# Kernel tuning notes

Hardware: AMD Instinct MI355X
Metric: run time of the kernel (lower is better)

The kernel has to match this reference:

```python
import jax, jax.numpy as jnp
import numpy as np

P = 64       # number of pathways
NV = 512     # features per pathway (nvar[i])
W = 256      # hidden width per pathway
COV = 16     # covariates
B = 2048     # batch
EPS = 1e-5   # BatchNorm eps
SLOPE = 0.2  # LeakyReLU negative slope


def _lrelu(v):
    return jnp.where(v >= 0, v, SLOPE * v)


def setup_inputs() -> dict:
    key = jax.random.key(0)
    ks = jax.random.split(key, 8)
    x = jax.random.normal(ks[0], (B, P * NV + COV), dtype=jnp.float32)
    # per-pathway weights (no bias), stacked across pathways -> grouped GEMM
    W1 = jax.random.normal(ks[1], (P, NV, W), dtype=jnp.float32) * (1.0 / np.sqrt(NV))
    W2 = jax.random.normal(ks[2], (P, W, W), dtype=jnp.float32) * (1.0 / np.sqrt(W))
    W3 = jax.random.normal(ks[3], (P, W), dtype=jnp.float32) * (1.0 / np.sqrt(W))
    gamma = jnp.ones((P,), dtype=jnp.float32)   # bn_path weight
    beta = jnp.zeros((P,), dtype=jnp.float32)   # bn_path bias
    fc_w = jax.random.normal(ks[4], (P + COV, 1), dtype=jnp.float32) * 0.05
    fc_b = jnp.full((1,), 0.001, dtype=jnp.float32)
    return {"x": x, "W1": W1, "W2": W2, "W3": W3,
            "gamma": gamma, "beta": beta, "fc_w": fc_w, "fc_b": fc_b}


def reference(x, W1, W2, W3, gamma, beta, fc_w, fc_b):
    # pathway blocks (dropout = identity in eval): grouped GEMMs over P pathways
    xp = x[:, : P * NV].reshape(B, P, NV)
    h = _lrelu(jnp.einsum('bpi,pio->bpo', xp, W1))
    h = _lrelu(jnp.einsum('bpi,pio->bpo', h, W2))
    p = _lrelu(jnp.einsum('bpi,pi->bp', h, W3))          # [B, P]
    # BatchNorm1d (training-mode batch statistics, biased variance)
    mean = p.mean(axis=0)
    var = p.var(axis=0)
    pn = (p - mean) / jnp.sqrt(var + EPS) * gamma + beta
    # global L2 (Frobenius) normalization, as torch.norm(pathway_layer, 2)
    pn = pn / jnp.linalg.norm(pn)
    # concat covariates, final linear + sigmoid
    z = jnp.concatenate([pn, x[:, P * NV: P * NV + COV]], axis=1)  # [B, P+COV]
    return jax.nn.sigmoid(z @ fc_w + fc_b)                         # [B, 1]
```

## Files before the change

### kernel.cpp

```cpp
#include <hip/hip_runtime.h>
#include <hip/hip_bf16.h>

#define PW 64
#define NV 512
#define HW 256
#define COV 16
#define BATCH 2048
#define XROW (PW * NV + COV)

typedef short s16x8 __attribute__((ext_vector_type(8)));
typedef float f32x4 __attribute__((ext_vector_type(4)));

__device__ __forceinline__ unsigned short f2bf(float f) {
    union { float f; unsigned int u; } v;
    v.f = f;
    unsigned int u = v.u;
    unsigned int r = (u + 0x7fffu + ((u >> 16) & 1u)) >> 16;
    return (unsigned short)r;
}

__device__ __forceinline__ unsigned int pack2(float a, float b) {
    __hip_bfloat162 h = __float22bfloat162_rn(float2{a, b});
    union { __hip_bfloat162 h; unsigned int u; } c;
    c.h = h;
    return c.u;
}

__global__ __launch_bounds__(256)
void transpose_all(const float* __restrict__ W1, const float* __restrict__ W2,
                   unsigned short* __restrict__ W1T, unsigned short* __restrict__ W2T) {
    __shared__ float tile[32][33];
    const float* in;
    unsigned short* out;
    int R, C, c0, r0, p;
    int bx = blockIdx.x;
    if (bx < 8192) {
        R = NV; C = HW;
        c0 = (bx & 7) * 32;
        r0 = ((bx >> 3) & 15) * 32;
        p  = bx >> 7;
        in = W1; out = W1T;
    } else {
        bx -= 8192;
        R = HW; C = HW;
        c0 = (bx & 7) * 32;
        r0 = ((bx >> 3) & 7) * 32;
        p  = bx >> 6;
        in = W2; out = W2T;
    }
    const float* ip = in + (size_t)p * R * C;
    unsigned short* op = out + (size_t)p * R * C;
    const int tx = threadIdx.x & 31;
    const int ty = threadIdx.x >> 5;
    #pragma unroll
    for (int j = 0; j < 32; j += 8)
        tile[ty + j][tx] = ip[(size_t)(r0 + ty + j) * C + c0 + tx];
    __syncthreads();
    #pragma unroll
    for (int j = 0; j < 32; j += 8)
        op[(size_t)(c0 + ty + j) * R + r0 + tx] = f2bf(tile[tx][ty + j]);
}

template<int K, bool CONV_A, bool FUSE>
__global__ __launch_bounds__(256)
void gemm_fused(const void* __restrict__ Abase, const unsigned short* __restrict__ BT,
                unsigned short* __restrict__ Hout, const float* __restrict__ W3,
                float* __restrict__ pvec, int lda, long aPs) {
    __shared__ __align__(16) unsigned short As[128][72];
    __shared__ __align__(16) unsigned short Bs[256][72];
    __shared__ float red[2][128];

    const int p   = blockIdx.z;
    const int bm0 = blockIdx.x * 128;
    const int t    = threadIdx.x;
    const int lane = t & 63;
    const int wave = t >> 6;
    const int wm  = (wave & 1) * 64;
    const int wni = wave >> 1;
    const int wn  = wni * 128;
    const int l15  = lane & 15;
    const int quad = lane >> 4;

    f32x4 acc[4][8] = {};

    const unsigned short* Bp = BT + (size_t)p * HW * K;

    for (int k0 = 0; k0 < K; k0 += 64) {
        if (CONV_A) {
            const float* Ap = (const float*)Abase + (size_t)p * aPs;
            #pragma unroll
            for (int i = 0; i < 8; ++i) {
                int idx = t + i * 256;
                int row = idx >> 4;
                int c4  = (idx & 15) * 4;
                float4 v = *(const float4*)(Ap + (size_t)(bm0 + row) * lda + k0 + c4);
                uint2 u;
                u.x = pack2(v.x, v.y);
                u.y = pack2(v.z, v.w);
                *(uint2*)&As[row][c4] = u;
            }
        } else {
            const unsigned short* Ap = (const unsigned short*)Abase + (size_t)p * aPs;
            #pragma unroll
            for (int i = 0; i < 4; ++i) {
                int idx = t + i * 256;
                int row = idx >> 3;
                int c8  = (idx & 7) * 8;
                *(s16x8*)&As[row][c8] = *(const s16x8*)(Ap + (size_t)(bm0 + row) * lda + k0 + c8);
            }
        }
        #pragma unroll
        for (int i = 0; i < 8; ++i) {
            int idx = t + i * 256;
            int row = idx >> 3;
            int c8  = (idx & 7) * 8;
            *(s16x8*)&Bs[row][c8] = *(const s16x8*)(Bp + (size_t)row * K + k0 + c8);
        }
        __syncthreads();

        #pragma unroll
        for (int kk = 0; kk < 64; kk += 32) {
            s16x8 af[4], bfr[8];
            #pragma unroll
            for (int mi = 0; mi < 4; ++mi)
                af[mi] = *(const s16x8*)&As[wm + mi * 16 + l15][kk + quad * 8];
            #pragma unroll
            for (int ni = 0; ni < 8; ++ni)
                bfr[ni] = *(const s16x8*)&Bs[wn + ni * 16 + l15][kk + quad * 8];
            #pragma unroll
            for (int mi = 0; mi < 4; ++mi)
                #pragma unroll
                for (int ni = 0; ni < 8; ++ni)
                    acc[mi][ni] = __builtin_amdgcn_mfma_f32_16x16x32_bf16(
                        af[mi], bfr[ni], acc[mi][ni], 0, 0, 0);
        }
        __syncthreads();
    }

    if (!FUSE) {
        unsigned short* Cp = Hout + (size_t)p * BATCH * HW;
        #pragma unroll
        for (int mi = 0; mi < 4; ++mi) {
            #pragma unroll
            for (int ni = 0; ni < 8; ++ni) {
                int col = wn + ni * 16 + l15;
                #pragma unroll
                for (int r = 0; r < 4; ++r) {
                    int row = bm0 + wm + mi * 16 + quad * 4 + r;
                    float v = acc[mi][ni][r];
                    v = v >= 0.f ? v : 0.2f * v;
                    Cp[(size_t)row * HW + col] = f2bf(v);
                }
            }
        }
    } else {
        float w3v[8];
        #pragma unroll
        for (int ni = 0; ni < 8; ++ni)
            w3v[ni] = W3[(size_t)p * HW + wn + ni * 16 + l15];
        float part[4][4];
        #pragma unroll
        for (int mi = 0; mi < 4; ++mi) {
            #pragma unroll
            for (int r = 0; r < 4; ++r) {
                float s = 0.f;
                #pragma unroll
                for (int ni = 0; ni < 8; ++ni) {
                    float v = acc[mi][ni][r];
                    v = v >= 0.f ? v : 0.2f * v;
                    s += v * w3v[ni];
                }
                part[mi][r] = s;
            }
        }
        #pragma unroll
        for (int off = 1; off < 16; off <<= 1)
            #pragma unroll
            for (int mi = 0; mi < 4; ++mi)
                #pragma unroll
                for (int r = 0; r < 4; ++r)
                    part[mi][r] += __shfl_xor(part[mi][r], off);
        if (l15 == 0) {
            #pragma unroll
            for (int mi = 0; mi < 4; ++mi)
                #pragma unroll
                for (int r = 0; r < 4; ++r)
                    red[wni][wm + mi * 16 + quad * 4 + r] = part[mi][r];
        }
        __syncthreads();
        if (t < 128) {
            float s = red[0][t] + red[1][t];
            s = s >= 0.f ? s : 0.2f * s;
            pvec[(size_t)p * BATCH + bm0 + t] = s;
        }
    }
}

__global__ __launch_bounds__(1024)
void stats_all(const float* __restrict__ pvec, const float* __restrict__ gamma,
               const float* __restrict__ beta, float* __restrict__ stat) {
    __shared__ float sm[64], sq[64];
    const int wave = threadIdx.x >> 6;
    const int lane = threadIdx.x & 63;
    #pragma unroll
    for (int pp = 0; pp < 4; ++pp) {
        const int p = wave * 4 + pp;
        float s = 0.f, q = 0.f;
        for (int i = lane; i < BATCH; i += 64) {
            float v = pvec[(size_t)p * BATCH + i];
            s += v; q += v * v;
        }
        #pragma unroll
        for (int off = 32; off; off >>= 1) {
            s += __shfl_down(s, off);
            q += __shfl_down(q, off);
        }
        if (lane == 0) { sm[p] = s; sq[p] = q; }
    }
    __syncthreads();
    if (threadIdx.x < 64) {
        const int p = threadIdx.x;
        float mean = sm[p] * (1.f / BATCH);
        float var  = sq[p] * (1.f / BATCH) - mean * mean;
        float invstd = rsqrtf(var + 1e-5f);
        stat[p]      = mean;
        stat[64 + p] = invstd;
        float g = gamma[p], bt = beta[p];
        float contrib = (float)BATCH * (g * g * var / (var + 1e-5f) + bt * bt);
        #pragma unroll
        for (int off = 32; off; off >>= 1) contrib += __shfl_down(contrib, off);
        if (p == 0) stat[128] = rsqrtf(contrib);
    }
}

__global__ __launch_bounds__(256)
void final_k(const float* __restrict__ pvec, const float* __restrict__ stat,
             const float* __restrict__ gamma, const float* __restrict__ beta,
             const float* __restrict__ x, const float* __restrict__ fc_w,
             const float* __restrict__ fc_b, float* __restrict__ out) {
    const int b = blockIdx.x * 256 + threadIdx.x;
    const float rn = stat[128];
    float acc = fc_b[0];
    #pragma unroll
    for (int p = 0; p < PW; ++p) {
        float pn = (pvec[(size_t)p * BATCH + b] - stat[p]) * stat[64 + p] * gamma[p] + beta[p];
        acc += pn * rn * fc_w[p];
    }
    #pragma unroll
    for (int c = 0; c < COV; ++c)
        acc += x[(size_t)b * XROW + PW * NV + c] * fc_w[PW + c];
    out[b] = 1.f / (1.f + __expf(-acc));
}

extern "C" void kernel_launch(void* const* d_in, const int* in_sizes, int n_in,
                              void* d_out, int out_size, void* d_ws, size_t ws_size,
                              hipStream_t stream) {
    const float* x     = (const float*)d_in[0];
    const float* W1    = (const float*)d_in[1];
    const float* W2    = (const float*)d_in[2];
    const float* W3    = (const float*)d_in[3];
    const float* gamma = (const float*)d_in[4];
    const float* beta  = (const float*)d_in[5];
    const float* fc_w  = (const float*)d_in[6];
    const float* fc_b  = (const float*)d_in[7];
    float* out = (float*)d_out;

    char* ws = (char*)d_ws;
    size_t off = 0;
    unsigned short* W1T = (unsigned short*)(ws + off); off += (size_t)PW * NV * HW * 2;
    unsigned short* W2T = (unsigned short*)(ws + off); off += (size_t)PW * HW * HW * 2;
    unsigned short* H1  = (unsigned short*)(ws + off); off += (size_t)PW * BATCH * HW * 2;
    float* pvec = (float*)(ws + off); off += (size_t)PW * BATCH * 4;
    float* stat = (float*)(ws + off); off += 256 * 4;

    transpose_all<<<dim3(8192 + 4096), 256, 0, stream>>>(W1, W2, W1T, W2T);

    gemm_fused<NV, true, false><<<dim3(BATCH / 128, 1, PW), 256, 0, stream>>>(
        (const void*)x, W1T, H1, nullptr, nullptr, XROW, (long)NV);

    gemm_fused<HW, false, true><<<dim3(BATCH / 128, 1, PW), 256, 0, stream>>>(
        (const void*)H1, W2T, nullptr, W3, pvec, HW, (long)BATCH * HW);

    stats_all<<<1, 1024, 0, stream>>>(pvec, gamma, beta, stat);

    final_k<<<BATCH / 256, 256, 0, stream>>>(pvec, stat, gamma, beta, x, fc_w, fc_b, out);
}
```

Measured before the change: 541.4 us.

## Fuse both pathway GEMMs into one kernel keeping H1 in shared memory

```diff
diff --git a/kernel.cpp b/kernel.cpp
--- a/kernel.cpp
+++ b/kernel.cpp
@@ -25,6 +25,8 @@
     c.h = h;
     return c.u;
 }
+
+__device__ __forceinline__ float lrelu(float v) { return v >= 0.f ? v : 0.2f * v; }
 
 __global__ __launch_bounds__(256)
 void transpose_all(const float* __restrict__ W1, const float* __restrict__ W2,
@@ -61,175 +63,169 @@
         op[(size_t)(c0 + ty + j) * R + r0 + tx] = f2bf(tile[tx][ty + j]);
 }
 
-template<int K, bool CONV_A, bool FUSE>
-__global__ __launch_bounds__(256)
-void gemm_fused(const void* __restrict__ Abase, const unsigned short* __restrict__ BT,
-                unsigned short* __restrict__ Hout, const float* __restrict__ W3,
-                float* __restrict__ pvec, int lda, long aPs) {
-    __shared__ __align__(16) unsigned short As[128][72];
+__global__ __launch_bounds__(256, 2)
+void pathway_fused(const float* __restrict__ x, const unsigned short* __restrict__ W1T,
+                   const unsigned short* __restrict__ W2T, const float* __restrict__ W3,
+                   float* __restrict__ pvec) {
+    __shared__ __align__(16) unsigned short As[64][72];
     __shared__ __align__(16) unsigned short Bs[256][72];
-    __shared__ float red[2][128];
-
-    const int p   = blockIdx.z;
-    const int bm0 = blockIdx.x * 128;
+    __shared__ __align__(16) unsigned short H1t[64][264];
+    __shared__ float red[4][64];
+
+    const int bm0 = blockIdx.x * 64;
+    const int p   = blockIdx.y;
     const int t    = threadIdx.x;
     const int lane = t & 63;
     const int wave = t >> 6;
-    const int wm  = (wave & 1) * 64;
-    const int wni = wave >> 1;
-    const int wn  = wni * 128;
+    const int wn   = wave * 64;
     const int l15  = lane & 15;
     const int quad = lane >> 4;
 
-    f32x4 acc[4][8] = {};
-
-    const unsigned short* Bp = BT + (size_t)p * HW * K;
-
-    for (int k0 = 0; k0 < K; k0 += 64) {
-        if (CONV_A) {
-            const float* Ap = (const float*)Abase + (size_t)p * aPs;
-            #pragma unroll
-            for (int i = 0; i < 8; ++i) {
+    const float* Ap          = x   + (size_t)p * NV;
+    const unsigned short* B1 = W1T + (size_t)p * HW * NV;
+    const unsigned short* B2 = W2T + (size_t)p * HW * HW;
+
+    {
+        f32x4 acc[4][4] = {};
+        for (int k0 = 0; k0 < NV; k0 += 64) {
+            #pragma unroll
+            for (int i = 0; i < 4; ++i) {
                 int idx = t + i * 256;
                 int row = idx >> 4;
                 int c4  = (idx & 15) * 4;
-                float4 v = *(const float4*)(Ap + (size_t)(bm0 + row) * lda + k0 + c4);
+                float4 v = *(const float4*)(Ap + (size_t)(bm0 + row) * XROW + k0 + c4);
                 uint2 u;
                 u.x = pack2(v.x, v.y);
                 u.y = pack2(v.z, v.w);
                 *(uint2*)&As[row][c4] = u;
             }
-        } else {
-            const unsigned short* Ap = (const unsigned short*)Abase + (size_t)p * aPs;
-            #pragma unroll
-            for (int i = 0; i < 4; ++i) {
+            #pragma unroll
+            for (int i = 0; i < 8; ++i) {
                 int idx = t + i * 256;
                 int row = idx >> 3;
                 int c8  = (idx & 7) * 8;
-                *(s16x8*)&As[row][c8] = *(const s16x8*)(Ap + (size_t)(bm0 + row) * lda + k0 + c8);
+                *(s16x8*)&Bs[row][c8] = *(const s16x8*)(B1 + (size_t)row * NV + k0 + c8);
             }
-        }
+            __syncthreads();
+            #pragma unroll
+            for (int kk = 0; kk < 64; kk += 32) {
+                s16x8 af[4], bfr[4];
+                #pragma unroll
+                for (int mi = 0; mi < 4; ++mi)
+                    af[mi] = *(const s16x8*)&As[mi * 16 + l15][kk + quad * 8];
+                #pragma unroll
+                for (int ni = 0; ni < 4; ++ni)
+                    bfr[ni] = *(const s16x8*)&Bs[wn + ni * 16 + l15][kk + quad * 8];
+                #pragma unroll
+                for (int mi = 0; mi < 4; ++mi)
+                    #pragma unroll
+                    for (int ni = 0; ni < 4; ++ni)
+                        acc[mi][ni] = __builtin_amdgcn_mfma_f32_16x16x32_bf16(
+                            af[mi], bfr[ni], acc[mi][ni], 0, 0, 0);
+            }
+            __syncthreads();
+        }
+        #pragma unroll
+        for (int mi = 0; mi < 4; ++mi)
+            #pragma unroll
+            for (int ni = 0; ni < 4; ++ni)
+                #pragma unroll
+                for (int r = 0; r < 4; ++r)
+                    H1t[mi * 16 + quad * 4 + r][wn + ni * 16 + l15] =
+                        f2bf(lrelu(acc[mi][ni][r]));
+    }
+    __syncthreads();
+
+    f32x4 acc2[4][4] = {};
+    for (int k0 = 0; k0 < HW; k0 += 64) {
         #pragma unroll
         for (int i = 0; i < 8; ++i) {
             int idx = t + i * 256;
             int row = idx >> 3;
             int c8  = (idx & 7) * 8;
-            *(s16x8*)&Bs[row][c8] = *(const s16x8*)(Bp + (size_t)row * K + k0 + c8);
+            *(s16x8*)&Bs[row][c8] = *(const s16x8*)(B2 + (size_t)row * HW + k0 + c8);
         }
         __syncthreads();
-
         #pragma unroll
         for (int kk = 0; kk < 64; kk += 32) {
-            s16x8 af[4], bfr[8];
+            s16x8 af[4], bfr[4];
             #pragma unroll
             for (int mi = 0; mi < 4; ++mi)
-                af[mi] = *(const s16x8*)&As[wm + mi * 16 + l15][kk + quad * 8];
-            #pragma unroll
-            for (int ni = 0; ni < 8; ++ni)
+                af[mi] = *(const s16x8*)&H1t[mi * 16 + l15][k0 + kk + quad * 8];
+            #pragma unroll
+            for (int ni = 0; ni < 4; ++ni)
                 bfr[ni] = *(const s16x8*)&Bs[wn + ni * 16 + l15][kk + quad * 8];
             #pragma unroll
             for (int mi = 0; mi < 4; ++mi)
                 #pragma unroll
-                for (int ni = 0; ni < 8; ++ni)
-                    acc[mi][ni] = __builtin_amdgcn_mfma_f32_16x16x32_bf16(
-                        af[mi], bfr[ni], acc[mi][ni], 0, 0, 0);
+                for (int ni = 0; ni < 4; ++ni)
+                    acc2[mi][ni] = __builtin_amdgcn_mfma_f32_16x16x32_bf16(
+                        af[mi], bfr[ni], acc2[mi][ni], 0, 0, 0);
         }
         __syncthreads();
     }
 
-    if (!FUSE) {
-        unsigned short* Cp = Hout + (size_t)p * BATCH * HW;
-        #pragma unroll
-        for (int mi = 0; mi < 4; ++mi) {
-            #pragma unroll
-            for (int ni = 0; ni < 8; ++ni) {
-                int col = wn + ni * 16 + l15;
-                #pragma unroll
-                for (int r = 0; r < 4; ++r) {
-                    int row = bm0 + wm + mi * 16 + quad * 4 + r;
-                    float v = acc[mi][ni][r];
-                    v = v >= 0.f ? v : 0.2f * v;
-                    Cp[(size_t)row * HW + col] = f2bf(v);
-                }
-            }
-        }
-    } else {
-        float w3v[8];
-        #pragma unroll
-        for (int ni = 0; ni < 8; ++ni)
-            w3v[ni] = W3[(size_t)p * HW + wn + ni * 16 + l15];
-        float part[4][4];
-        #pragma unroll
-        for (int mi = 0; mi < 4; ++mi) {
-            #pragma unroll
-            for (int r = 0; r < 4; ++r) {
-                float s = 0.f;
-                #pragma unroll
-                for (int ni = 0; ni < 8; ++ni) {
-                    float v = acc[mi][ni][r];
-                    v = v >= 0.f ? v : 0.2f * v;
-                    s += v * w3v[ni];
-                }
-                part[mi][r] = s;
-            }
-        }
-        #pragma unroll
-        for (int off = 1; off < 16; off <<= 1)
-            #pragma unroll
-            for (int mi = 0; mi < 4; ++mi)
-                #pragma unroll
-                for (int r = 0; r < 4; ++r)
-                    part[mi][r] += __shfl_xor(part[mi][r], off);
-        if (l15 == 0) {
-            #pragma unroll
-            for (int mi = 0; mi < 4; ++mi)
-                #pragma unroll
-                for (int r = 0; r < 4; ++r)
-                    red[wni][wm + mi * 16 + quad * 4 + r] = part[mi][r];
-        }
-        __syncthreads();
-        if (t < 128) {
-            float s = red[0][t] + red[1][t];
-            s = s >= 0.f ? s : 0.2f * s;
-            pvec[(size_t)p * BATCH + bm0 + t] = s;
-        }
-    }
-}
-
-__global__ __launch_bounds__(1024)
-void stats_all(const float* __restrict__ pvec, const float* __restrict__ gamma,
-               const float* __restrict__ beta, float* __restrict__ stat) {
-    __shared__ float sm[64], sq[64];
-    const int wave = threadIdx.x >> 6;
-    const int lane = threadIdx.x & 63;
-    #pragma unroll
-    for (int pp = 0; pp < 4; ++pp) {
-        const int p = wave * 4 + pp;
-        float s = 0.f, q = 0.f;
-        for (int i = lane; i < BATCH; i += 64) {
-            float v = pvec[(size_t)p * BATCH + i];
-            s += v; q += v * v;
-        }
-        #pragma unroll
-        for (int off = 32; off; off >>= 1) {
-            s += __shfl_down(s, off);
-            q += __shfl_down(q, off);
-        }
-        if (lane == 0) { sm[p] = s; sq[p] = q; }
-    }
-    __syncthreads();
-    if (threadIdx.x < 64) {
-        const int p = threadIdx.x;
-        float mean = sm[p] * (1.f / BATCH);
-        float var  = sq[p] * (1.f / BATCH) - mean * mean;
-        float invstd = rsqrtf(var + 1e-5f);
-        stat[p]      = mean;
-        stat[64 + p] = invstd;
-        float g = gamma[p], bt = beta[p];
-        float contrib = (float)BATCH * (g * g * var / (var + 1e-5f) + bt * bt);
-        #pragma unroll
-        for (int off = 32; off; off >>= 1) contrib += __shfl_down(contrib, off);
-        if (p == 0) stat[128] = rsqrtf(contrib);
+    float w3v[4];
+    #pragma unroll
+    for (int ni = 0; ni < 4; ++ni)
+        w3v[ni] = W3[(size_t)p * HW + wn + ni * 16 + l15];
+    float part[4][4];
+    #pragma unroll
+    for (int mi = 0; mi < 4; ++mi) {
+        #pragma unroll
+        for (int r = 0; r < 4; ++r) {
+            float s = 0.f;
+            #pragma unroll
+            for (int ni = 0; ni < 4; ++ni)
+                s += lrelu(acc2[mi][ni][r]) * w3v[ni];
+            part[mi][r] = s;
+        }
+    }
+    #pragma unroll
+    for (int off = 1; off < 16; off <<= 1)
+        #pragma unroll
+        for (int mi = 0; mi < 4; ++mi)
+            #pragma unroll
+            for (int r = 0; r < 4; ++r)
+                part[mi][r] += __shfl_xor(part[mi][r], off);
+    if (l15 == 0)
+        #pragma unroll
+        for (int mi = 0; mi < 4; ++mi)
+            #pragma unroll
+            for (int r = 0; r < 4; ++r)
+                red[wave][mi * 16 + quad * 4 + r] = part[mi][r];
+    __syncthreads();
+    if (t < 64) {
+        float s = red[0][t] + red[1][t] + red[2][t] + red[3][t];
+        pvec[(size_t)p * BATCH + bm0 + t] = lrelu(s);
+    }
+}
+
+__global__ __launch_bounds__(256)
+void stats_k(const float* __restrict__ pvec, float* __restrict__ stat) {
+    const int p = blockIdx.x;
+    float s = 0.f, q = 0.f;
+    for (int i = threadIdx.x; i < BATCH; i += 256) {
+        float v = pvec[(size_t)p * BATCH + i];
+        s += v; q += v * v;
+    }
+    #pragma unroll
+    for (int off = 32; off; off >>= 1) {
+        s += __shfl_down(s, off);
+        q += __shfl_down(q, off);
+    }
+    __shared__ float ls[4], lq[4];
+    const int wave = threadIdx.x >> 6, lane = threadIdx.x & 63;
+    if (lane == 0) { ls[wave] = s; lq[wave] = q; }
+    __syncthreads();
+    if (threadIdx.x == 0) {
+        float S = ls[0] + ls[1] + ls[2] + ls[3];
+        float Q = lq[0] + lq[1] + lq[2] + lq[3];
+        float mean = S * (1.f / BATCH);
+        float var  = Q * (1.f / BATCH) - mean * mean;
+        stat[p]       = mean;
+        stat[64 + p]  = rsqrtf(var + 1e-5f);
+        stat[128 + p] = var;
     }
 }
 
@@ -239,7 +235,13 @@
              const float* __restrict__ x, const float* __restrict__ fc_w,
              const float* __restrict__ fc_b, float* __restrict__ out) {
     const int b = blockIdx.x * 256 + threadIdx.x;
-    const float rn = stat[128];
+    float nsq = 0.f;
+    #pragma unroll
+    for (int p = 0; p < PW; ++p) {
+        float g = gamma[p], bt = beta[p], var = stat[128 + p], inv = stat[64 + p];
+        nsq += (float)BATCH * (g * g * var * inv * inv + bt * bt);
+    }
+    const float rn = rsqrtf(nsq);
     float acc = fc_b[0];
     #pragma unroll
     for (int p = 0; p < PW; ++p) {
@@ -269,19 +271,14 @@
     size_t off = 0;
     unsigned short* W1T = (unsigned short*)(ws + off); off += (size_t)PW * NV * HW * 2;
     unsigned short* W2T = (unsigned short*)(ws + off); off += (size_t)PW * HW * HW * 2;
-    unsigned short* H1  = (unsigned short*)(ws + off); off += (size_t)PW * BATCH * HW * 2;
     float* pvec = (float*)(ws + off); off += (size_t)PW * BATCH * 4;
     float* stat = (float*)(ws + off); off += 256 * 4;
 
     transpose_all<<<dim3(8192 + 4096), 256, 0, stream>>>(W1, W2, W1T, W2T);
 
-    gemm_fused<NV, true, false><<<dim3(BATCH / 128, 1, PW), 256, 0, stream>>>(
-        (const void*)x, W1T, H1, nullptr, nullptr, XROW, (long)NV);
-
-    gemm_fused<HW, false, true><<<dim3(BATCH / 128, 1, PW), 256, 0, stream>>>(
-        (const void*)H1, W2T, nullptr, W3, pvec, HW, (long)BATCH * HW);
-
-    stats_all<<<1, 1024, 0, stream>>>(pvec, gamma, beta, stat);
+    pathway_fused<<<dim3(BATCH / 64, PW), 256, 0, stream>>>(x, W1T, W2T, W3, pvec);
+
+    stats_k<<<PW, 256, 0, stream>>>(pvec, stat);
 
     final_k<<<BATCH / 256, 256, 0, stream>>>(pvec, stat, gamma, beta, x, fc_w, fc_b, out);
 }
```

Measured after the change: 461.1 us. -14.8%, faster.
